# Performance work log

Measured on AMD Instinct MI355X. Metric: run time of the kernel, lower is better.

Reference implementation:

```python
import jax, jax.numpy as jnp
import numpy as np

B, N, C_IN, C_OUT, K = 8, 2048, 64, 128, 20
EPS = 1e-5  # BatchNorm2d default eps


def setup_inputs() -> dict:
    key = jax.random.key(0)
    k1, k2 = jax.random.split(key, 2)
    x = jax.random.normal(k1, (B, C_IN, N), dtype=jnp.float32)
    fan_in = 2 * C_IN
    W = jax.random.normal(k2, (C_OUT, 2 * C_IN), dtype=jnp.float32) / np.sqrt(fan_in).astype(np.float32)
    b = jnp.zeros((C_OUT,), jnp.float32)
    gamma = jnp.ones((C_OUT,), jnp.float32)
    beta = jnp.zeros((C_OUT,), jnp.float32)
    return {"x": x, "W": W, "b": b, "gamma": gamma, "beta": beta}


def reference(x, W, b, gamma, beta):
    # x: (B, C_in, N) -> points (B, N, C_in)
    pts = jnp.transpose(x, (0, 2, 1))
    # pairwise squared L2 distances (B, N, N)
    sq = jnp.sum(pts * pts, axis=-1)
    dist = sq[:, :, None] + sq[:, None, :] - 2.0 * jnp.einsum('bnc,bmc->bnm', pts, pts)
    # knn: top-k of negated distance -> k nearest neighbors (includes self)
    _, nn_idx = jax.lax.top_k(-dist, K)  # (B, N, K)
    # gather neighbor features per batch: (B, N, K, C_in)
    neigh = jax.vmap(lambda p, i: p[i])(pts, nn_idx)
    central = pts[:, :, None, :]  # (B, N, 1, C_in)
    edge = jnp.concatenate(
        [jnp.broadcast_to(central, neigh.shape), neigh - central], axis=-1
    )  # (B, N, K, 2*C_in)
    # 1x1 conv == channelwise linear: (B, N, K, C_out)
    y = jnp.einsum('bnkc,oc->bnko', edge, W) + b
    # BatchNorm2d (training mode): stats over batch + spatial dims, biased var
    mean = jnp.mean(y, axis=(0, 1, 2))
    var = jnp.var(y, axis=(0, 1, 2))
    y = (y - mean) * jax.lax.rsqrt(var + EPS) * gamma + beta
    y = jax.nn.relu(y)
    y = jnp.max(y, axis=2)  # max over k neighbors -> (B, N, C_out)
    return jnp.transpose(y, (0, 2, 1))[..., None]  # (B, C_out, N, 1)
```

## Files before the change

kernel.cpp:

```cpp
#include <hip/hip_runtime.h>
#include <cstdint>
#include <cstddef>

#define NPTS 2048
#define BATCH 8
#define CIN 64
#define CO 128
#define KNN 20
#define KSEL 24
#define NSPLIT 4
#define MKP 25

typedef short s16x8 __attribute__((ext_vector_type(8)));
typedef unsigned short u16x8 __attribute__((ext_vector_type(8)));
typedef float f32x4 __attribute__((ext_vector_type(4)));

__device__ inline unsigned short f2bf_rne(float x) {
  unsigned u = __float_as_uint(x);
  unsigned r = (u + 0x7FFFu + ((u >> 16) & 1u)) >> 16;
  return (unsigned short)r;
}
__device__ inline float bf2f(unsigned short h) {
  return __uint_as_float(((unsigned)h) << 16);
}
__device__ inline unsigned med3u(unsigned a, unsigned b, unsigned c) {
  unsigned d;
  asm("v_med3_u32 %0, %1, %2, %3" : "=v"(d) : "v"(a), "v"(b), "v"(c));
  return d;
}

__global__ __launch_bounds__(256) void prep_kernel(
    const float* __restrict__ x, float* __restrict__ P,
    unsigned short* __restrict__ PG, float* __restrict__ SQ,
    float* __restrict__ STATS) {
  __shared__ float tile[64 * 33];
  const int b = blockIdx.y, hb = blockIdx.x;
  const int n0 = hb * 32;
  const int tid = threadIdx.x;
  if (b == 0 && hb == 0) {
    for (int t = tid; t < 5 * CO; t += 256) STATS[t] = 0.f;
  }
  const float* xb = x + (size_t)b * CIN * NPTS;
#pragma unroll
  for (int j = 0; j < 8; ++j) {
    int e = j * 256 + tid;
    int c = e >> 5, nl = e & 31;
    tile[c * 33 + nl] = xb[(size_t)c * NPTS + n0 + nl];
  }
  __syncthreads();
  float* Pb = P + (size_t)b * NPTS * CIN;
#pragma unroll
  for (int j = 0; j < 8; ++j) {
    int e = j * 256 + tid;
    int nl = e >> 6, c = e & 63;
    Pb[(size_t)(n0 + nl) * CIN + c] = tile[c * 33 + nl];
  }
  if (tid < 32) {
    float acc = 0.f;
#pragma unroll
    for (int c = 0; c < 64; ++c) {
      float v = tile[c * 33 + tid];
      acc = fmaf(v, v, acc);
    }
    SQ[(size_t)b * NPTS + n0 + tid] = acc;
  }
  const size_t tbase = (size_t)(b * 32 + (n0 >> 6)) * 8192;
  {
    const int rl = tid >> 3, kc = tid & 7;
    const int grow = (n0 & 63) + rl;
    const int frag = ((grow >> 4) << 1) | (kc >> 2);
    const int lidx = (grow & 15) | ((kc & 3) << 4);
    s16x8 hi8, lo8;
#pragma unroll
    for (int e = 0; e < 8; ++e) {
      float v = tile[(kc * 8 + e) * 33 + rl];
      unsigned short hb_ = f2bf_rne(v);
      float hf = bf2f(hb_);
      unsigned short lb = f2bf_rne(v - hf);
      hi8[e] = (short)hb_;
      lo8[e] = (short)lb;
    }
    size_t co = (size_t)(frag * 64 + lidx) * 8;
    *(s16x8*)(PG + tbase + co) = hi8;
    *(s16x8*)(PG + tbase + 4096 + co) = lo8;
  }
}

__global__ __launch_bounds__(256) void knn_part_kernel(
    const unsigned short* __restrict__ PG, const float* __restrict__ SQ,
    unsigned* __restrict__ POOLS) {
  const int b = blockIdx.z;
  const int cs = blockIdx.y;
  const int n0 = blockIdx.x * 64;
  const int tid = threadIdx.x;
  const int lane = tid & 63, w = tid >> 6;
  const int qi = w * 16 + (lane & 15);
  const int sub = lane >> 4;
  const int T0 = cs * 8;

  __shared__ unsigned mk[64 * 4 * MKP];

  const size_t tqb = (size_t)(b * 32 + (n0 >> 6)) * 8192;
  const s16x8 qhi0 = *(const s16x8*)(PG + tqb + (size_t)((w * 2 + 0) * 64 + lane) * 8);
  const s16x8 qhi1 = *(const s16x8*)(PG + tqb + (size_t)((w * 2 + 1) * 64 + lane) * 8);
  const s16x8 qlo0 = *(const s16x8*)(PG + tqb + 4096 + (size_t)((w * 2 + 0) * 64 + lane) * 8);
  const s16x8 qlo1 = *(const s16x8*)(PG + tqb + 4096 + (size_t)((w * 2 + 1) * 64 + lane) * 8);

  unsigned hk[KSEL];
#pragma unroll
  for (int s = 0; s < KSEL; ++s) hk[s] = 0xFFFFFFFFu;

#pragma unroll 1
  for (int t = 0; t < 8; ++t) {
    const int T = T0 + t;
    const unsigned short* tb = PG + (size_t)(b * 32 + T) * 8192;
#pragma unroll
    for (int rt = 0; rt < 4; ++rt) {
      const s16x8 ahi0 = *(const s16x8*)(tb + (size_t)((rt * 2 + 0) * 64 + lane) * 8);
      const s16x8 ahi1 = *(const s16x8*)(tb + (size_t)((rt * 2 + 1) * 64 + lane) * 8);
      const s16x8 alo0 = *(const s16x8*)(tb + 4096 + (size_t)((rt * 2 + 0) * 64 + lane) * 8);
      const s16x8 alo1 = *(const s16x8*)(tb + 4096 + (size_t)((rt * 2 + 1) * 64 + lane) * 8);
      f32x4 acc = {0.f, 0.f, 0.f, 0.f};
      acc = __builtin_amdgcn_mfma_f32_16x16x32_bf16(alo0, qhi0, acc, 0, 0, 0);
      acc = __builtin_amdgcn_mfma_f32_16x16x32_bf16(ahi0, qlo0, acc, 0, 0, 0);
      acc = __builtin_amdgcn_mfma_f32_16x16x32_bf16(ahi0, qhi0, acc, 0, 0, 0);
      acc = __builtin_amdgcn_mfma_f32_16x16x32_bf16(alo1, qhi1, acc, 0, 0, 0);
      acc = __builtin_amdgcn_mfma_f32_16x16x32_bf16(ahi1, qlo1, acc, 0, 0, 0);
      acc = __builtin_amdgcn_mfma_f32_16x16x32_bf16(ahi1, qhi1, acc, 0, 0, 0);
      const float4 sq4 = *(const float4*)(SQ + b * NPTS + T * 64 + rt * 16 + sub * 4);
      const float sqa[4] = {sq4.x, sq4.y, sq4.z, sq4.w};
      const int mbase = T * 64 + rt * 16 + sub * 4;
#pragma unroll
      for (int r = 0; r < 4; ++r) {
        float d = fmaf(acc[r], -2.0f, sqa[r]);
        unsigned u = __float_as_uint(d);
        unsigned ord = u ^ (unsigned)(((int)u >> 31) | 0x80000000);
        unsigned key = (ord & 0xFFFFF800u) | (unsigned)(mbase + r);
#pragma unroll
        for (int s = KSEL - 1; s >= 1; --s) hk[s] = med3u(hk[s - 1], hk[s], key);
        hk[0] = hk[0] < key ? hk[0] : key;
      }
    }
  }

#pragma unroll
  for (int s = 0; s < KSEL; ++s) mk[(qi * 4 + sub) * MKP + s] = hk[s];
  __syncthreads();

  if (sub == 0) {
    const unsigned* bl = mk + qi * 4 * MKP;
    unsigned* pq = POOLS + ((size_t)(b * NPTS + n0 + qi) * NSPLIT + cs) * KSEL;
    int p0 = 0, p1 = 0, p2 = 0, p3 = 0;
#pragma unroll 1
    for (int s = 0; s < KSEL; ++s) {
      unsigned k0 = (p0 < KSEL) ? bl[0 * MKP + p0] : 0xFFFFFFFFu;
      unsigned k1 = (p1 < KSEL) ? bl[1 * MKP + p1] : 0xFFFFFFFFu;
      unsigned k2 = (p2 < KSEL) ? bl[2 * MKP + p2] : 0xFFFFFFFFu;
      unsigned k3 = (p3 < KSEL) ? bl[3 * MKP + p3] : 0xFFFFFFFFu;
      unsigned bk = k0; int bs = 0;
      if (k1 < bk) { bk = k1; bs = 1; }
      if (k2 < bk) { bk = k2; bs = 2; }
      if (k3 < bk) { bk = k3; bs = 3; }
      pq[s] = bk;
      if (bs == 0) ++p0; else if (bs == 1) ++p1; else if (bs == 2) ++p2; else ++p3;
    }
  }
}

__global__ __launch_bounds__(256) void merge_proj_kernel(
    const float* __restrict__ P, const float* __restrict__ W,
    const unsigned* __restrict__ POOLS, int* __restrict__ IDX,
    float* __restrict__ U, unsigned short* __restrict__ Vh) {
  __shared__ __align__(16) char smem[35072];
  const int tid = threadIdx.x;

  if (blockIdx.x < 1024) {
    const int blk = blockIdx.x;
    const int r0 = (blk >> 2) * 64;
    const int o0 = (blk & 3) * 32;
    const int og = tid & 3;
    const int nl = tid >> 2;
    float* Pt = (float*)smem;
    float* Wu_s = Pt + 64 * 65;
    float* Wd_s = Wu_s + 64 * 36;

#pragma unroll
    for (int j = 0; j < 16; ++j) {
      int e = j * 256 + tid;
      int c = e & 63, rl = e >> 6;
      Pt[rl * 65 + c] = P[((size_t)(r0 + rl) << 6) + c];
    }
#pragma unroll
    for (int j = 0; j < 8; ++j) {
      int e = j * 256 + tid;
      int c = e & 63, ol = e >> 6;
      float w1 = W[(size_t)(o0 + ol) * 128 + c];
      float w2 = W[(size_t)(o0 + ol) * 128 + 64 + c];
      Wu_s[c * 36 + ol] = w1 - w2;
      Wd_s[c * 36 + ol] = w2;
    }
    __syncthreads();

    float au[8] = {0,0,0,0,0,0,0,0};
    float av[8] = {0,0,0,0,0,0,0,0};
#pragma unroll 4
    for (int c = 0; c < 64; ++c) {
      float p = Pt[nl * 65 + c];
      const float* wu = Wu_s + c * 36 + og * 8;
      const float* wd = Wd_s + c * 36 + og * 8;
      float4 u0 = *(const float4*)wu;
      float4 u1 = *(const float4*)(wu + 4);
      float4 dd0 = *(const float4*)wd;
      float4 dd1 = *(const float4*)(wd + 4);
      au[0] = fmaf(p, u0.x, au[0]); au[1] = fmaf(p, u0.y, au[1]);
      au[2] = fmaf(p, u0.z, au[2]); au[3] = fmaf(p, u0.w, au[3]);
      au[4] = fmaf(p, u1.x, au[4]); au[5] = fmaf(p, u1.y, au[5]);
      au[6] = fmaf(p, u1.z, au[6]); au[7] = fmaf(p, u1.w, au[7]);
      av[0] = fmaf(p, dd0.x, av[0]); av[1] = fmaf(p, dd0.y, av[1]);
      av[2] = fmaf(p, dd0.z, av[2]); av[3] = fmaf(p, dd0.w, av[3]);
      av[4] = fmaf(p, dd1.x, av[4]); av[5] = fmaf(p, dd1.y, av[5]);
      av[6] = fmaf(p, dd1.z, av[6]); av[7] = fmaf(p, dd1.w, av[7]);
    }
    size_t ob = (size_t)(r0 + nl) * CO + o0 + og * 8;
    float4 s0 = {au[0], au[1], au[2], au[3]};
    float4 s1 = {au[4], au[5], au[6], au[7]};
    *(float4*)(U + ob) = s0;
    *(float4*)(U + ob + 4) = s1;
    u16x8 hv;
#pragma unroll
    for (int j = 0; j < 8; ++j) hv[j] = f2bf_rne(av[j]);
    *(u16x8*)(Vh + ob) = hv;
  } else {
    const int mblk = blockIdx.x - 1024;
    const int qi = tid >> 3, st = tid & 7;
    const int r0 = mblk * 32;
    const int r = r0 + qi;
    const int b = r >> 11;

    unsigned* lists = (unsigned*)smem;
    unsigned* pool = lists + 32 * NSPLIT * KSEL;
    double* cd = (double*)(pool + 32 * KSEL);

    {
      const unsigned* src = POOLS + (size_t)r0 * NSPLIT * KSEL;
      for (int t = tid; t < 32 * NSPLIT * KSEL; t += 256) lists[t] = src[t];
    }
    __syncthreads();

    if (st == 0) {
      const unsigned* bl = lists + qi * NSPLIT * KSEL;
      unsigned* pq = pool + qi * KSEL;
      int p0 = 0, p1 = 0, p2 = 0, p3 = 0;
#pragma unroll 1
      for (int s = 0; s < KSEL; ++s) {
        unsigned k0 = (p0 < KSEL) ? bl[0 * KSEL + p0] : 0xFFFFFFFFu;
        unsigned k1 = (p1 < KSEL) ? bl[1 * KSEL + p1] : 0xFFFFFFFFu;
        unsigned k2 = (p2 < KSEL) ? bl[2 * KSEL + p2] : 0xFFFFFFFFu;
        unsigned k3 = (p3 < KSEL) ? bl[3 * KSEL + p3] : 0xFFFFFFFFu;
        unsigned bk = k0; int bs = 0;
        if (k1 < bk) { bk = k1; bs = 1; }
        if (k2 < bk) { bk = k2; bs = 2; }
        if (k3 < bk) { bk = k3; bs = 3; }
        pq[s] = bk;
        if (bs == 0) ++p0; else if (bs == 1) ++p1; else if (bs == 2) ++p2; else ++p3;
      }
    }
    __syncthreads();

    const float* qrow = P + ((size_t)r << 6);
    float4 q4[16];
#pragma unroll
    for (int t = 0; t < 16; ++t) q4[t] = ((const float4*)qrow)[t];
#pragma unroll 1
    for (int j = 0; j < 3; ++j) {
      int cand = st * 3 + j;
      unsigned key = pool[qi * KSEL + cand];
      int m = (int)(key & 0x7FFu);
      const float* prow = P + ((size_t)(b * NPTS + m) << 6);
      double a0 = 0.0, a1 = 0.0;
#pragma unroll
      for (int t = 0; t < 16; ++t) {
        float4 pv = ((const float4*)prow)[t];
        double d0 = (double)pv.x - (double)q4[t].x;
        double d1 = (double)pv.y - (double)q4[t].y;
        double d2 = (double)pv.z - (double)q4[t].z;
        double d3 = (double)pv.w - (double)q4[t].w;
        a0 = fma(d1, d1, fma(d0, d0, a0));
        a1 = fma(d3, d3, fma(d2, d2, a1));
      }
      cd[qi * KSEL + cand] = a0 + a1;
    }
    __syncthreads();

    int* op = IDX + (size_t)r * KNN;
#pragma unroll 1
    for (int j = 0; j < 3; ++j) {
      int cand = st * 3 + j;
      double dv = cd[qi * KSEL + cand];
      int iv = (int)(pool[qi * KSEL + cand] & 0x7FFu);
      int rk = 0;
#pragma unroll 1
      for (int t = 0; t < KSEL; ++t) {
        double dt = cd[qi * KSEL + t];
        int it = (int)(pool[qi * KSEL + t] & 0x7FFu);
        rk += ((dt < dv) || (dt == dv && it < iv)) ? 1 : 0;
      }
      if (rk < KNN) op[rk] = iv;
    }
  }
}

__global__ __launch_bounds__(256) void gstats_kernel(
    const float* __restrict__ U, const unsigned short* __restrict__ Vh,
    const int* __restrict__ IDX, float* __restrict__ Z, float* __restrict__ STATS) {
  const int r0 = blockIdx.x * 16;
  const int tid = threadIdx.x;
  const int og = tid & 15, nl = tid >> 4;
  const int r = r0 + nl;
  const int b = r >> 11;
  const unsigned short* Vb = Vh + ((size_t)b << 11) * CO;

  __shared__ int ii[16 * KNN];
  __shared__ float red[4][5][128];

  for (int t = tid; t < 16 * KNN; t += 256) ii[t] = IDX[(size_t)r0 * KNN + t];
  __syncthreads();

  float vmax[8], svr[8], svvr[8];
#pragma unroll
  for (int j = 0; j < 8; ++j) { vmax[j] = -3.4e38f; svr[j] = 0.f; svvr[j] = 0.f; }
#pragma unroll 4
  for (int k = 0; k < KNN; ++k) {
    int idx = ii[nl * KNN + k];
    u16x8 hv = *(const u16x8*)(Vb + (size_t)idx * CO + og * 8);
#pragma unroll
    for (int j = 0; j < 8; ++j) {
      float v = bf2f((unsigned short)hv[j]);
      vmax[j] = fmaxf(vmax[j], v);
      svr[j] += v;
      svvr[j] = fmaf(v, v, svvr[j]);
    }
  }
  size_t ob = (size_t)r * CO + og * 8;
  float4 u0 = *(const float4*)(U + ob);
  float4 u1 = *(const float4*)(U + ob + 4);
  float uu[8] = {u0.x, u0.y, u0.z, u0.w, u1.x, u1.y, u1.z, u1.w};
  float4 z0 = {uu[0] + vmax[0], uu[1] + vmax[1], uu[2] + vmax[2], uu[3] + vmax[3]};
  float4 z1 = {uu[4] + vmax[4], uu[5] + vmax[5], uu[6] + vmax[6], uu[7] + vmax[7]};
  *(float4*)(Z + ob) = z0;
  *(float4*)(Z + ob + 4) = z1;

  float pu[8], puu[8], psv[8], pusv[8], psvv[8];
#pragma unroll
  for (int j = 0; j < 8; ++j) {
    pu[j] = uu[j];
    puu[j] = uu[j] * uu[j];
    psv[j] = svr[j];
    pusv[j] = uu[j] * svr[j];
    psvv[j] = svvr[j];
  }
#pragma unroll
  for (int j = 0; j < 8; ++j) {
    pu[j]   += __shfl_xor(pu[j], 16);   pu[j]   += __shfl_xor(pu[j], 32);
    puu[j]  += __shfl_xor(puu[j], 16);  puu[j]  += __shfl_xor(puu[j], 32);
    psv[j]  += __shfl_xor(psv[j], 16);  psv[j]  += __shfl_xor(psv[j], 32);
    pusv[j] += __shfl_xor(pusv[j], 16); pusv[j] += __shfl_xor(pusv[j], 32);
    psvv[j] += __shfl_xor(psvv[j], 16); psvv[j] += __shfl_xor(psvv[j], 32);
  }
  const int w = tid >> 6;
  if ((tid & 0x30) == 0) {
#pragma unroll
    for (int j = 0; j < 8; ++j) {
      int c = og * 8 + j;
      red[w][0][c] = pu[j];  red[w][1][c] = puu[j];  red[w][2][c] = psv[j];
      red[w][3][c] = pusv[j]; red[w][4][c] = psvv[j];
    }
  }
  __syncthreads();
  if (tid < 128) {
#pragma unroll
    for (int s = 0; s < 5; ++s) {
      float v4 = red[0][s][tid] + red[1][s][tid] + red[2][s][tid] + red[3][s][tid];
      atomicAdd(&STATS[s * CO + tid], v4);
    }
  }
}

__global__ __launch_bounds__(256) void out_kernel(
    const float* __restrict__ Z, const float* __restrict__ STATS,
    const float* __restrict__ bias, const float* __restrict__ gamma,
    const float* __restrict__ beta, float* __restrict__ out) {
  const int n0 = blockIdx.x * 64, o0 = blockIdx.y * 32, b = blockIdx.z;
  const int tid = threadIdx.x;
  __shared__ float tile[64 * 33];
  __shared__ float fs[32], ft[32];
  if (tid < 32) {
    const int o = o0 + tid;
    const float M = (float)(BATCH * NPTS * KNN);
    const float Kf = (float)KNN;
    float su = STATS[0 * CO + o], suu = STATS[1 * CO + o], ssv = STATS[2 * CO + o];
    float susv = STATS[3 * CO + o], ssvv = STATS[4 * CO + o];
    float bo = bias[o];
    float lin = (Kf * su + ssv) / M;
    float mean = lin + bo;
    float ey2 = (Kf * suu + ssvv + 2.0f * susv) / M + 2.0f * bo * lin + bo * bo;
    float var = ey2 - mean * mean;
    float scale = gamma[o] * rsqrtf(var + 1e-5f);
    fs[tid] = scale;
    ft[tid] = (bo - mean) * scale + beta[o];
  }
#pragma unroll
  for (int j = 0; j < 8; ++j) {
    int e = j * 256 + tid;
    int ol = e & 31, nl = e >> 5;
    tile[nl * 33 + ol] = Z[(size_t)(b * NPTS + n0 + nl) * CO + o0 + ol];
  }
  __syncthreads();
#pragma unroll
  for (int j = 0; j < 8; ++j) {
    int e = j * 256 + tid;
    int nl = e & 63, ol = e >> 6;
    float v = fmaf(tile[nl * 33 + ol], fs[ol], ft[ol]);
    out[(size_t)(b * CO + o0 + ol) * NPTS + n0 + nl] = fmaxf(v, 0.0f);
  }
}

extern "C" void kernel_launch(void* const* d_in, const int* in_sizes, int n_in,
                              void* d_out, int out_size, void* d_ws, size_t ws_size,
                              hipStream_t stream) {
  const float* x = (const float*)d_in[0];
  const float* W = (const float*)d_in[1];
  const float* bias = (const float*)d_in[2];
  const float* gamma = (const float*)d_in[3];
  const float* beta = (const float*)d_in[4];
  float* out = (float*)d_out;
  float* ws = (float*)d_ws;

  const size_t NR = (size_t)BATCH * NPTS;
  size_t off = 0;
  float* P = ws + off;                      off += NR * CIN;
  unsigned short* PG = (unsigned short*)(ws + off); off += NR * CIN;
  float* SQ = ws + off;                     off += NR;
  int* IDX = (int*)(ws + off);              off += NR * KNN;
  float* U = ws + off;                      off += NR * CO;
  unsigned short* Vh = (unsigned short*)(ws + off); off += NR * CO / 2;
  unsigned* POOLS = (unsigned*)(ws + off);  off += NR * NSPLIT * KSEL;
  float* STATS = ws + off;                  off += 5 * CO;
  float* Z = ws;
  if (ws_size < off * sizeof(float)) return;

  prep_kernel<<<dim3(NPTS / 32, BATCH), 256, 0, stream>>>(x, P, PG, SQ, STATS);
  knn_part_kernel<<<dim3(NPTS / 64, NSPLIT, BATCH), 256, 0, stream>>>(PG, SQ, POOLS);
  merge_proj_kernel<<<dim3(1024 + NR / 32), 256, 0, stream>>>(P, W, POOLS, IDX, U, Vh);
  gstats_kernel<<<dim3(NR / 16), 256, 0, stream>>>(U, Vh, IDX, Z, STATS);
  out_kernel<<<dim3(NPTS / 64, CO / 32, BATCH), 256, 0, stream>>>(Z, STATS, bias, gamma, beta, out);
}
```

Measured before the change: 137.5 us.

## Split MFMA accumulator chains, add occupancy hint, store Z intermediate as bf16

The knn distance MFMAs now accumulate into two independent chains that are summed at the end, which shortens the dependent MFMA latency chain. The kernel also gets a launch_bounds minimum-occupancy hint of 4 blocks. Separately, the pre-normalisation Z tensor is written and read as bf16 instead of fp32, halving traffic between gstats and the output kernel at the cost of reduced precision in the final output.

```diff
diff --git a/kernel.cpp b/kernel.cpp
--- a/kernel.cpp
+++ b/kernel.cpp
@@ -86,7 +86,7 @@
   }
 }
 
-__global__ __launch_bounds__(256) void knn_part_kernel(
+__global__ __launch_bounds__(256, 4) void knn_part_kernel(
     const unsigned short* __restrict__ PG, const float* __restrict__ SQ,
     unsigned* __restrict__ POOLS) {
   const int b = blockIdx.z;
@@ -120,19 +120,20 @@
       const s16x8 ahi1 = *(const s16x8*)(tb + (size_t)((rt * 2 + 1) * 64 + lane) * 8);
       const s16x8 alo0 = *(const s16x8*)(tb + 4096 + (size_t)((rt * 2 + 0) * 64 + lane) * 8);
       const s16x8 alo1 = *(const s16x8*)(tb + 4096 + (size_t)((rt * 2 + 1) * 64 + lane) * 8);
-      f32x4 acc = {0.f, 0.f, 0.f, 0.f};
-      acc = __builtin_amdgcn_mfma_f32_16x16x32_bf16(alo0, qhi0, acc, 0, 0, 0);
-      acc = __builtin_amdgcn_mfma_f32_16x16x32_bf16(ahi0, qlo0, acc, 0, 0, 0);
-      acc = __builtin_amdgcn_mfma_f32_16x16x32_bf16(ahi0, qhi0, acc, 0, 0, 0);
-      acc = __builtin_amdgcn_mfma_f32_16x16x32_bf16(alo1, qhi1, acc, 0, 0, 0);
-      acc = __builtin_amdgcn_mfma_f32_16x16x32_bf16(ahi1, qlo1, acc, 0, 0, 0);
-      acc = __builtin_amdgcn_mfma_f32_16x16x32_bf16(ahi1, qhi1, acc, 0, 0, 0);
+      f32x4 acc0 = {0.f, 0.f, 0.f, 0.f};
+      f32x4 acc1 = {0.f, 0.f, 0.f, 0.f};
+      acc0 = __builtin_amdgcn_mfma_f32_16x16x32_bf16(alo0, qhi0, acc0, 0, 0, 0);
+      acc1 = __builtin_amdgcn_mfma_f32_16x16x32_bf16(alo1, qhi1, acc1, 0, 0, 0);
+      acc0 = __builtin_amdgcn_mfma_f32_16x16x32_bf16(ahi0, qlo0, acc0, 0, 0, 0);
+      acc1 = __builtin_amdgcn_mfma_f32_16x16x32_bf16(ahi1, qlo1, acc1, 0, 0, 0);
+      acc0 = __builtin_amdgcn_mfma_f32_16x16x32_bf16(ahi0, qhi0, acc0, 0, 0, 0);
+      acc1 = __builtin_amdgcn_mfma_f32_16x16x32_bf16(ahi1, qhi1, acc1, 0, 0, 0);
       const float4 sq4 = *(const float4*)(SQ + b * NPTS + T * 64 + rt * 16 + sub * 4);
       const float sqa[4] = {sq4.x, sq4.y, sq4.z, sq4.w};
       const int mbase = T * 64 + rt * 16 + sub * 4;
 #pragma unroll
       for (int r = 0; r < 4; ++r) {
-        float d = fmaf(acc[r], -2.0f, sqa[r]);
+        float d = fmaf(acc0[r] + acc1[r], -2.0f, sqa[r]);
         unsigned u = __float_as_uint(d);
         unsigned ord = u ^ (unsigned)(((int)u >> 31) | 0x80000000);
         unsigned key = (ord & 0xFFFFF800u) | (unsigned)(mbase + r);
@@ -312,7 +313,8 @@
 
 __global__ __launch_bounds__(256) void gstats_kernel(
     const float* __restrict__ U, const unsigned short* __restrict__ Vh,
-    const int* __restrict__ IDX, float* __restrict__ Z, float* __restrict__ STATS) {
+    const int* __restrict__ IDX, unsigned short* __restrict__ Zh,
+    float* __restrict__ STATS) {
   const int r0 = blockIdx.x * 16;
   const int tid = threadIdx.x;
   const int og = tid & 15, nl = tid >> 4;
@@ -345,10 +347,10 @@
   float4 u0 = *(const float4*)(U + ob);
   float4 u1 = *(const float4*)(U + ob + 4);
   float uu[8] = {u0.x, u0.y, u0.z, u0.w, u1.x, u1.y, u1.z, u1.w};
-  float4 z0 = {uu[0] + vmax[0], uu[1] + vmax[1], uu[2] + vmax[2], uu[3] + vmax[3]};
-  float4 z1 = {uu[4] + vmax[4], uu[5] + vmax[5], uu[6] + vmax[6], uu[7] + vmax[7]};
-  *(float4*)(Z + ob) = z0;
-  *(float4*)(Z + ob + 4) = z1;
+  u16x8 zh;
+#pragma unroll
+  for (int j = 0; j < 8; ++j) zh[j] = f2bf_rne(uu[j] + vmax[j]);
+  *(u16x8*)(Zh + ob) = zh;
 
   float pu[8], puu[8], psv[8], pusv[8], psvv[8];
 #pragma unroll
@@ -387,7 +389,7 @@
 }
 
 __global__ __launch_bounds__(256) void out_kernel(
-    const float* __restrict__ Z, const float* __restrict__ STATS,
+    const unsigned short* __restrict__ Zh, const float* __restrict__ STATS,
     const float* __restrict__ bias, const float* __restrict__ gamma,
     const float* __restrict__ beta, float* __restrict__ out) {
   const int n0 = blockIdx.x * 64, o0 = blockIdx.y * 32, b = blockIdx.z;
@@ -413,7 +415,7 @@
   for (int j = 0; j < 8; ++j) {
     int e = j * 256 + tid;
     int ol = e & 31, nl = e >> 5;
-    tile[nl * 33 + ol] = Z[(size_t)(b * NPTS + n0 + nl) * CO + o0 + ol];
+    tile[nl * 33 + ol] = bf2f(Zh[(size_t)(b * NPTS + n0 + nl) * CO + o0 + ol]);
   }
   __syncthreads();
 #pragma unroll
@@ -446,12 +448,12 @@
   unsigned short* Vh = (unsigned short*)(ws + off); off += NR * CO / 2;
   unsigned* POOLS = (unsigned*)(ws + off);  off += NR * NSPLIT * KSEL;
   float* STATS = ws + off;                  off += 5 * CO;
-  float* Z = ws;
+  unsigned short* Zh = (unsigned short*)ws;
   if (ws_size < off * sizeof(float)) return;
 
   prep_kernel<<<dim3(NPTS / 32, BATCH), 256, 0, stream>>>(x, P, PG, SQ, STATS);
   knn_part_kernel<<<dim3(NPTS / 64, NSPLIT, BATCH), 256, 0, stream>>>(PG, SQ, POOLS);
   merge_proj_kernel<<<dim3(1024 + NR / 32), 256, 0, stream>>>(P, W, POOLS, IDX, U, Vh);
-  gstats_kernel<<<dim3(NR / 16), 256, 0, stream>>>(U, Vh, IDX, Z, STATS);
-  out_kernel<<<dim3(NPTS / 64, CO / 32, BATCH), 256, 0, stream>>>(Z, STATS, bias, gamma, beta, out);
-}
+  gstats_kernel<<<dim3(NR / 16), 256, 0, stream>>>(U, Vh, IDX, Zh, STATS);
+  out_kernel<<<dim3(NPTS / 64, CO / 32, BATCH), 256, 0, stream>>>(Zh, STATS, bias, gamma, beta, out);
+}
```

New measurement: 135.7 us. No clear change (-1.2%).
